# Kernel optimization log

Hardware: AMD Instinct MI355X
Metric: run time of the kernel (lower is better)

## Reference

```python
import jax, jax.numpy as jnp
import numpy as np

INPUT_SIZE = 1024
HIDDEN_SIZE = 1024
BATCH = 8192
MLP_H1, MLP_H2 = 16, 8


def _uniform(key, shape, stdv):
    return jax.random.uniform(key, shape, jnp.float32, -stdv, stdv)


def setup_inputs() -> dict:
    key = jax.random.key(0)
    ks = jax.random.split(key, 20)
    stdv = 1.0 / np.sqrt(HIDDEN_SIZE)
    I, H = INPUT_SIZE, HIDDEN_SIZE
    inp = {
        "x": jax.random.normal(ks[0], (BATCH, I), jnp.float32),
        "h": jax.random.normal(ks[1], (BATCH, H), jnp.float32),
        "c": jax.random.normal(ks[2], (BATCH, H), jnp.float32),
        # gate weights (torch layout: matmul(h, W_h*) + matmul(x, W_x*) + b)
        "W_hi": _uniform(ks[3], (H, H), stdv),
        "W_xi": _uniform(ks[4], (I, H), stdv),
        "b_i": _uniform(ks[5], (H,), stdv),
        "W_hc": _uniform(ks[6], (H, H), stdv),
        "W_xc": _uniform(ks[7], (I, H), stdv),
        "b_c": _uniform(ks[8], (H,), stdv),
        "W_ho": _uniform(ks[9], (H, H), stdv),
        "W_xo": _uniform(ks[10], (I, H), stdv),
        "b_o": _uniform(ks[11], (H,), stdv),
        # forget MLP: (I+H) -> 16 -> 8 -> H, ReLU hidden, sigmoid output
        "W1": _uniform(ks[12], (I + H, MLP_H1), stdv),
        "b1": _uniform(ks[13], (MLP_H1,), stdv),
        "W2": _uniform(ks[14], (MLP_H1, MLP_H2), stdv),
        "b2": _uniform(ks[15], (MLP_H2,), stdv),
        "W3": _uniform(ks[16], (MLP_H2, H), stdv),
        "b3": _uniform(ks[17], (H,), stdv),
    }
    return inp


def reference(x, h, c, W_hi, W_xi, b_i, W_hc, W_xc, b_c, W_ho, W_xo, b_o,
              W1, b1, W2, b2, W3, b3):
    # forget gate via small MLP on concat(x, h)
    xh = jnp.concatenate((x, h), axis=1)           # [B, I+H]
    z = jax.nn.relu(xh @ W1 + b1)                  # [B, 16]
    z = jax.nn.relu(z @ W2 + b2)                   # [B, 8]
    f = jax.nn.sigmoid(z @ W3 + b3)                # [B, H]

    i = jax.nn.sigmoid(h @ W_hi + x @ W_xi + b_i)
    g = jnp.tanh(h @ W_hc + x @ W_xc + b_c)
    o = jax.nn.sigmoid(h @ W_ho + x @ W_xo + b_o)

    c_new = f * c + i * g
    h_new = o * jnp.tanh(c_new)
    return (h_new, c_new, f)
```

## Files before the change

kernel.cpp:

```cpp
#include <hip/hip_runtime.h>
#include <math.h>

#define BATCH 8192
#define HDIM  1024
#define KDIM  2048
#define NDIM  3072

typedef __attribute__((ext_vector_type(8))) short short8;
typedef __attribute__((ext_vector_type(4))) float floatx4;

__device__ __forceinline__ float b2f(unsigned short u) {
  union { unsigned int i; float f; } v; v.i = ((unsigned int)u) << 16; return v.f;
}
__device__ __forceinline__ unsigned short f2b(float f) {
  union { unsigned int i; float f; } v; v.f = f;
  unsigned int r = v.i + 0x7FFFu + ((v.i >> 16) & 1u);
  return (unsigned short)(r >> 16);
}
__device__ __forceinline__ float ldsel(const void* p, size_t i, int isbf) {
  return isbf ? b2f(((const unsigned short*)p)[i]) : ((const float*)p)[i];
}
__device__ __forceinline__ float sigf(float x) { return 1.0f / (1.0f + __expf(-x)); }
__device__ __forceinline__ float tanhfast(float x) {
  float a = __builtin_fabsf(x);
  float t = __expf(-2.f * a);
  float r = (1.f - t) / (1.f + t);
  return copysignf(r, x);
}

__device__ __forceinline__ int detect_bf(const void* x) {
  unsigned int w = ((const unsigned int*)x)[threadIdx.x & 63];
  unsigned short lo = (unsigned short)(w & 0xFFFFu);
  int e = (lo >> 7) & 0xFF;
  bool ok = (e >= 110 && e <= 135) || ((lo & 0x7FFFu) == 0);
  unsigned long long m = __ballot(ok);
  return (__popcll(m) >= 48) ? 1 : 0;
}

__device__ __forceinline__ void gld16(const void* g, void* l) {
  auto gp = reinterpret_cast<__attribute__((address_space(1))) unsigned int*>(
      (unsigned long long)g);
  auto lp = reinterpret_cast<__attribute__((address_space(3))) unsigned int*>(
      (unsigned long long)l);
  __builtin_amdgcn_global_load_lds(gp, lp, 16, 0, 0);
}

__device__ __forceinline__ short8 ld8bf(const void* p, size_t off, int isbf) {
  short8 r;
  if (isbf) {
    r = *(const short8*)((const unsigned short*)p + off);
  } else {
    const float* s = (const float*)p + off;
    float4 a = *(const float4*)(s);
    float4 b = *(const float4*)(s + 4);
    r[0]=(short)f2b(a.x); r[1]=(short)f2b(a.y); r[2]=(short)f2b(a.z); r[3]=(short)f2b(a.w);
    r[4]=(short)f2b(b.x); r[5]=(short)f2b(b.y); r[6]=(short)f2b(b.z); r[7]=(short)f2b(b.w);
  }
  return r;
}

__device__ __forceinline__ void ld8f(const void* p, size_t off, int isbf, float* o) {
  if (isbf) {
    short8 s = *(const short8*)((const unsigned short*)p + off);
#pragma unroll
    for (int j = 0; j < 8; ++j) o[j] = b2f((unsigned short)s[j]);
  } else {
    const float* s = (const float*)p + off;
    float4 a = *(const float4*)(s);
    float4 b = *(const float4*)(s + 4);
    o[0]=a.x; o[1]=a.y; o[2]=a.z; o[3]=a.w;
    o[4]=b.x; o[5]=b.y; o[6]=b.z; o[7]=b.w;
  }
}

__global__ __launch_bounds__(256) void k_pre(
    const void* __restrict__ x, const void* __restrict__ h,
    const void* __restrict__ W1, const void* __restrict__ b1,
    const void* __restrict__ W2, const void* __restrict__ b2,
    const void* __restrict__ wxi, const void* __restrict__ whi,
    const void* __restrict__ wxc, const void* __restrict__ whc,
    const void* __restrict__ wxo, const void* __restrict__ who,
    unsigned short* __restrict__ A, unsigned short* __restrict__ WT,
    float* __restrict__ z2) {
  __shared__ __align__(16) char smem[21888];
  const int isbf = detect_bf(x);
  const int tid = threadIdx.x;
  const int bx = blockIdx.x;

  if (bx < 512) {
    char* tAb = smem;
    char* tBb = smem + 8192;
    float* part = (float*)(smem + 16384);
    float* z1s  = (float*)(smem + 20736);
    const int m0 = bx * 16;
    const int lane = tid & 63;
    const int w = tid >> 6;
    const int q = lane >> 4;
    const int r = lane & 15;
    const int arow = tid >> 4;
    const int ak = (tid & 15) * 16;

    floatx4 acc = {0.f, 0.f, 0.f, 0.f};

    for (int ktile = 0; ktile < 8; ++ktile) {
      const int k0 = ktile * 256;
      const void* src = (k0 < 1024) ? x : h;
      const int klocal = (k0 & 1023) + ak;
      short8 v0 = ld8bf(src, (size_t)(m0 + arow) * 1024 + klocal, isbf);
      short8 v1 = ld8bf(src, (size_t)(m0 + arow) * 1024 + klocal + 8, isbf);
      float wv[16];
      if (isbf) {
        const unsigned short* s = (const unsigned short*)W1 + (size_t)(k0 + tid) * 16;
        short8 s0 = *(const short8*)(s);
        short8 s1 = *(const short8*)(s + 8);
#pragma unroll
        for (int j = 0; j < 8; ++j) { wv[j] = b2f((unsigned short)s0[j]);
                                      wv[8 + j] = b2f((unsigned short)s1[j]); }
      } else {
        const float* s = (const float*)W1 + (size_t)(k0 + tid) * 16;
        float4 a0 = *(const float4*)(s);
        float4 a1 = *(const float4*)(s + 4);
        float4 a2 = *(const float4*)(s + 8);
        float4 a3 = *(const float4*)(s + 12);
        wv[0]=a0.x; wv[1]=a0.y; wv[2]=a0.z; wv[3]=a0.w;
        wv[4]=a1.x; wv[5]=a1.y; wv[6]=a1.z; wv[7]=a1.w;
        wv[8]=a2.x; wv[9]=a2.y; wv[10]=a2.z; wv[11]=a2.w;
        wv[12]=a3.x; wv[13]=a3.y; wv[14]=a3.z; wv[15]=a3.w;
      }
      if (!isbf) {
        unsigned short* Ao = A + (size_t)(m0 + arow) * KDIM + k0 + ak;
        *(short8*)(Ao) = v0;
        *(short8*)(Ao + 8) = v1;
      }
      {
        const int base = arow * 512 + ak * 2;
        const int sw = (arow & 7) << 4;
        *(short8*)(tAb + ((base) ^ sw)) = v0;
        *(short8*)(tAb + ((base + 16) ^ sw)) = v1;
      }
#pragma unroll
      for (int j = 0; j < 16; ++j) {
        *(unsigned short*)(tBb + ((j * 512 + tid * 2) ^ ((j & 7) << 4))) = f2b(wv[j]);
      }
      __syncthreads();
#pragma unroll
      for (int s = 0; s < 2; ++s) {
        const int ks = (w * 2 + s) * 32 + q * 8;
        short8 af = *(const short8*)(tAb + ((r * 512 + ks * 2) ^ ((r & 7) << 4)));
        short8 bf = *(const short8*)(tBb + ((r * 512 + ks * 2) ^ ((r & 7) << 4)));
        acc = __builtin_amdgcn_mfma_f32_16x16x32_bf16(af, bf, acc, 0, 0, 0);
      }
      __syncthreads();
    }
#pragma unroll
    for (int t = 0; t < 4; ++t) part[(w * 16 + q * 4 + t) * 17 + r] = acc[t];
    __syncthreads();
    {
      const int row = tid >> 4;
      const int n = tid & 15;
      float s = part[(0 * 16 + row) * 17 + n] + part[(1 * 16 + row) * 17 + n] +
                part[(2 * 16 + row) * 17 + n] + part[(3 * 16 + row) * 17 + n] +
                ldsel(b1, (size_t)n, isbf);
      z1s[row * 17 + n] = fmaxf(s, 0.f);
    }
    __syncthreads();
    if (tid < 128) {
      const int row = tid >> 3;
      const int p = tid & 7;
      float s = ldsel(b2, (size_t)p, isbf);
#pragma unroll
      for (int nn = 0; nn < 16; ++nn)
        s += z1s[row * 17 + nn] * ldsel(W2, (size_t)nn * 8 + p, isbf);
      z2[(size_t)(m0 + row) * 8 + p] = fmaxf(s, 0.f);
    }
  } else {
    float (*tbuf)[65] = (float(*)[65])smem;
    const int b = bx - 512;
    const int mat = b >> 8;
    const int rem = b & 255;
    const int ti = rem >> 4;
    const int tj = rem & 15;
    const void* Ws[6] = {wxi, whi, wxc, whc, wxo, who};
    const void* W = Ws[mat];
    const int gt = mat >> 1;
    const int half = mat & 1;
    const int rrow = tid >> 3;
    const int c8 = (tid & 7) * 8;
#pragma unroll
    for (int it = 0; it < 2; ++it) {
      int row = it * 32 + rrow;
      size_t off = (size_t)(ti * 64 + row) * 1024 + tj * 64 + c8;
      if (isbf) {
        const unsigned short* s = (const unsigned short*)W + off;
        ushort4 a = *(const ushort4*)(s);
        ushort4 bv = *(const ushort4*)(s + 4);
        tbuf[row][c8+0]=b2f(a.x);  tbuf[row][c8+1]=b2f(a.y);
        tbuf[row][c8+2]=b2f(a.z);  tbuf[row][c8+3]=b2f(a.w);
        tbuf[row][c8+4]=b2f(bv.x); tbuf[row][c8+5]=b2f(bv.y);
        tbuf[row][c8+6]=b2f(bv.z); tbuf[row][c8+7]=b2f(bv.w);
      } else {
        const float* s = (const float*)W + off;
        float4 a = *(const float4*)(s);
        float4 bv = *(const float4*)(s + 4);
        tbuf[row][c8+0]=a.x;  tbuf[row][c8+1]=a.y;  tbuf[row][c8+2]=a.z;  tbuf[row][c8+3]=a.w;
        tbuf[row][c8+4]=bv.x; tbuf[row][c8+5]=bv.y; tbuf[row][c8+6]=bv.z; tbuf[row][c8+7]=bv.w;
      }
    }
    __syncthreads();
#pragma unroll
    for (int it = 0; it < 2; ++it) {
      int nl = it * 32 + rrow;
      int n = gt * 1024 + tj * 64 + nl;
      int kk = half * 1024 + ti * 64 + c8;
      short8 pk;
#pragma unroll
      for (int i = 0; i < 8; ++i) pk[i] = (short)f2b(tbuf[c8 + i][nl]);
      *(short8*)(WT + (size_t)n * KDIM + kk) = pk;
    }
  }
}

__global__ __launch_bounds__(256, 3) void k_gemm(
    const void* __restrict__ x, const void* __restrict__ h,
    const unsigned short* __restrict__ Apack,
    const unsigned short* __restrict__ WT,
    unsigned short* __restrict__ P) {
  const int isbf = detect_bf(x);
  const unsigned short* Ax = isbf ? (const unsigned short*)x : Apack;
  const unsigned short* Ah = isbf ? (const unsigned short*)h : (Apack + 1024);
  const int sA = isbf ? 1024 : 2048;
  __shared__ __align__(16) unsigned short lA[128 * 64];
  __shared__ __align__(16) unsigned short lB[128 * 64];
  const int tid = threadIdx.x;
  const int lane = tid & 63;
  const int wv = tid >> 6;
  const int wm = (wv >> 1) << 6;
  const int wn = (wv & 1) << 6;
  const int lin = blockIdx.y * 24 + blockIdx.x;
  const int swz = ((lin & 7) * 192) + (lin >> 3);
  const int m0 = (swz / 24) << 7;
  const int n0 = (swz % 24) << 7;

  floatx4 acc[4][4];
  const floatx4 fzero = {0.f, 0.f, 0.f, 0.f};
#pragma unroll
  for (int i = 0; i < 4; ++i)
#pragma unroll
    for (int j = 0; j < 4; ++j) acc[i][j] = fzero;

  int rr[4], kk[4];
#pragma unroll
  for (int ps = 0; ps < 4; ++ps) {
    int chunk = ps * 256 + tid;
    rr[ps] = chunk >> 3;
    kk[ps] = (chunk & 7) ^ (rr[ps] & 7);
  }
  const int px0 = (lane >> 4) ^ (lane & 7);
  const int px1 = ((lane >> 4) + 4) ^ (lane & 7);
  const int rowA = wm + (lane & 15);
  const int rowB = wn + (lane & 15);

  for (int kt = 0; kt < KDIM / 64; ++kt) {
    const int k0 = kt * 64;
    const unsigned short* Abase = (k0 < 1024) ? (Ax + k0) : (Ah + (k0 - 1024));
#pragma unroll
    for (int ps = 0; ps < 4; ++ps) {
      const int chunk = ps * 256 + tid;
      gld16(Abase + (size_t)(m0 + rr[ps]) * sA + kk[ps] * 8, lA + chunk * 8);
      gld16(WT + ((size_t)(n0 + rr[ps]) * KDIM + k0 + kk[ps] * 8), lB + chunk * 8);
    }
    __syncthreads();
#pragma unroll
    for (int s = 0; s < 2; ++s) {
      const int px = s ? px1 : px0;
      short8 af[4], bfr[4];
#pragma unroll
      for (int i = 0; i < 4; ++i)
        af[i] = *(const short8*)(lA + ((((rowA + (i << 4)) << 3) + px) << 3));
#pragma unroll
      for (int i = 0; i < 4; ++i)
        bfr[i] = *(const short8*)(lB + ((((rowB + (i << 4)) << 3) + px) << 3));
#pragma unroll
      for (int mi = 0; mi < 4; ++mi)
#pragma unroll
        for (int ni = 0; ni < 4; ++ni)
          acc[mi][ni] = __builtin_amdgcn_mfma_f32_16x16x32_bf16(
              af[mi], bfr[ni], acc[mi][ni], 0, 0, 0);
    }
    __syncthreads();
  }
  const int col = lane & 15;
  const int rq = (lane >> 4) << 2;
#pragma unroll
  for (int mi = 0; mi < 4; ++mi) {
#pragma unroll
    for (int ni = 0; ni < 4; ++ni) {
      const size_t n = (size_t)(n0 + wn + (ni << 4) + col);
#pragma unroll
      for (int t = 0; t < 4; ++t) {
        const size_t m = (size_t)(m0 + wm + (mi << 4) + rq + t);
        P[m * NDIM + n] = f2b(acc[mi][ni][t]);
      }
    }
  }
}

__global__ __launch_bounds__(256) void k_pointwise(
    const unsigned short* __restrict__ P, const void* __restrict__ x,
    const void* __restrict__ cin,
    const void* __restrict__ bi, const void* __restrict__ bc,
    const void* __restrict__ bo, const float* __restrict__ z2,
    const void* __restrict__ W3, const void* __restrict__ b3,
    void* __restrict__ out) {
  const int isbf = detect_bf(x);
  const int tid = threadIdx.x;
  const int n = (tid & 127) * 8;
  const int rhalf = tid >> 7;
  const size_t MH = (size_t)BATCH * HDIM;

  short8 w3p[8];
  float bif[8], bcf[8], bof[8], b3f[8];
  if (isbf) {
#pragma unroll
    for (int j = 0; j < 8; ++j)
      w3p[j] = *(const short8*)((const unsigned short*)W3 + j * 1024 + n);
  } else {
#pragma unroll
    for (int j = 0; j < 8; ++j) {
      const float* s = (const float*)W3 + j * 1024 + n;
      float4 a = *(const float4*)(s);
      float4 b = *(const float4*)(s + 4);
      short8 pk;
      pk[0]=(short)f2b(a.x); pk[1]=(short)f2b(a.y); pk[2]=(short)f2b(a.z); pk[3]=(short)f2b(a.w);
      pk[4]=(short)f2b(b.x); pk[5]=(short)f2b(b.y); pk[6]=(short)f2b(b.z); pk[7]=(short)f2b(b.w);
      w3p[j] = pk;
    }
  }
  ld8f(bi, (size_t)n, isbf, bif);
  ld8f(bc, (size_t)n, isbf, bcf);
  ld8f(bo, (size_t)n, isbf, bof);
  ld8f(b3, (size_t)n, isbf, b3f);

  const size_t mbase = (size_t)blockIdx.x * 4 + rhalf;
#pragma unroll
  for (int rI = 0; rI < 2; ++rI) {
    const size_t m = mbase + rI * 2;
    const size_t idx = m * HDIM + n;
    const unsigned short* pr = P + m * NDIM + n;
    short8 ui = *(const short8*)(pr);
    short8 ug = *(const short8*)(pr + 1024);
    short8 uo = *(const short8*)(pr + 2048);
    float4 za = *(const float4*)(z2 + m * 8);
    float4 zb = *(const float4*)(z2 + m * 8 + 4);
    float zz[8] = {za.x, za.y, za.z, za.w, zb.x, zb.y, zb.z, zb.w};
    float cf[8];
    ld8f(cin, idx, isbf, cf);
    float hn[8], cn[8], ff[8];
#pragma unroll
    for (int t = 0; t < 8; ++t) {
      float f3 = b3f[t];
#pragma unroll
      for (int j = 0; j < 8; ++j) f3 += zz[j] * b2f((unsigned short)w3p[j][t]);
      const float F = sigf(f3);
      const float I = sigf(b2f((unsigned short)ui[t]) + bif[t]);
      const float G = tanhfast(b2f((unsigned short)ug[t]) + bcf[t]);
      const float O = sigf(b2f((unsigned short)uo[t]) + bof[t]);
      const float C = F * cf[t] + I * G;
      ff[t] = F;
      cn[t] = C;
      hn[t] = O * tanhfast(C);
    }
    if (isbf) {
      unsigned short* ob = (unsigned short*)out;
      short8 ph, pc, pf;
#pragma unroll
      for (int t = 0; t < 8; ++t) {
        ph[t] = (short)f2b(hn[t]);
        pc[t] = (short)f2b(cn[t]);
        pf[t] = (short)f2b(ff[t]);
      }
      *(short8*)(ob + idx) = ph;
      *(short8*)(ob + MH + idx) = pc;
      *(short8*)(ob + 2 * MH + idx) = pf;
    } else {
      float* ob = (float*)out;
      *(float4*)(ob + idx)     = make_float4(hn[0], hn[1], hn[2], hn[3]);
      *(float4*)(ob + idx + 4) = make_float4(hn[4], hn[5], hn[6], hn[7]);
      *(float4*)(ob + MH + idx)     = make_float4(cn[0], cn[1], cn[2], cn[3]);
      *(float4*)(ob + MH + idx + 4) = make_float4(cn[4], cn[5], cn[6], cn[7]);
      *(float4*)(ob + 2 * MH + idx)     = make_float4(ff[0], ff[1], ff[2], ff[3]);
      *(float4*)(ob + 2 * MH + idx + 4) = make_float4(ff[4], ff[5], ff[6], ff[7]);
    }
  }
}

extern "C" void kernel_launch(void* const* d_in, const int* in_sizes, int n_in,
                              void* d_out, int out_size, void* d_ws, size_t ws_size,
                              hipStream_t stream) {
  const void* x    = d_in[0];
  const void* h    = d_in[1];
  const void* c    = d_in[2];
  const void* W_hi = d_in[3];
  const void* W_xi = d_in[4];
  const void* b_i  = d_in[5];
  const void* W_hc = d_in[6];
  const void* W_xc = d_in[7];
  const void* b_c  = d_in[8];
  const void* W_ho = d_in[9];
  const void* W_xo = d_in[10];
  const void* b_o  = d_in[11];
  const void* W1   = d_in[12];
  const void* b1   = d_in[13];
  const void* W2   = d_in[14];
  const void* b2   = d_in[15];
  const void* W3   = d_in[16];
  const void* b3   = d_in[17];

  char* ws = (char*)d_ws;
  unsigned short* A   = (unsigned short*)ws;
  unsigned short* WT  = (unsigned short*)(ws + 33554432);
  unsigned short* P   = (unsigned short*)(ws + 46137344);
  float*          z2b = (float*)(ws + 96468992);

  k_pre<<<dim3(2048), dim3(256), 0, stream>>>(x, h, W1, b1, W2, b2,
                                              W_xi, W_hi, W_xc, W_hc, W_xo, W_ho,
                                              A, WT, z2b);
  k_gemm<<<dim3(NDIM / 128, BATCH / 128), dim3(256), 0, stream>>>(x, h, A, WT, P);
  k_pointwise<<<dim3(BATCH / 4), dim3(256), 0, stream>>>(P, x, c, b_i, b_c, b_o,
                                                         z2b, W3, b3, d_out);
}
```

Baseline: 364.4 us.

## Pipeline GEMM with 4-stage LDS ring buffer and 256x128 tiles

The bf16 GEMM kernel now uses 512-thread blocks, each computing a 256x128 output tile. It streams 32-wide K slices through a 4-slot shared-memory ring, so global-to-LDS loads for future slices are issued while the MFMAs run on the current one. Explicit vmcnt waits, raw s_barrier and s_setprio replace the two __syncthreads per K step, and the LDS swizzle changes to match. This is meant to hide global load latency and cut synchronization stalls, at the cost of 96KB of LDS per block, lower occupancy, and dropping the previous block-index swizzle used for L2 locality.

```diff
diff --git a/kernel.cpp b/kernel.cpp
--- a/kernel.cpp
+++ b/kernel.cpp
@@ -220,26 +220,47 @@
   }
 }
 
-__global__ __launch_bounds__(256, 3) void k_gemm(
+__device__ __forceinline__ void stage_a(char* smem, const unsigned short* Ax,
+    const unsigned short* Ah, int sA, int m0, int tid, int n) {
+  const int kb = (n >> 1) * 64 + (n & 1) * 32;
+  const unsigned short* sp = (kb < 1024) ? (Ax + kb) : (Ah + (kb - 1024));
+#pragma unroll
+  for (int j = 0; j < 2; ++j) {
+    const int d = j * 512 + tid;
+    const int row = d >> 2;
+    const int q = (d & 3) ^ ((row >> 1) & 3);
+    gld16(sp + (size_t)(m0 + row) * sA + q * 8,
+          smem + ((n & 3) << 14) + d * 16);
+  }
+}
+__device__ __forceinline__ void stage_b(char* smem, const unsigned short* WT,
+    int n0, int tid, int n) {
+  const int kb = (n >> 1) * 64 + (n & 1) * 32;
+  const int row = tid >> 2;
+  const int q = (tid & 3) ^ ((row >> 1) & 3);
+  gld16(WT + (size_t)(n0 + row) * (size_t)KDIM + kb + q * 8,
+        smem + 65536 + ((n & 3) << 13) + tid * 16);
+}
+
+__global__ __launch_bounds__(512, 2) void k_gemm(
     const void* __restrict__ x, const void* __restrict__ h,
     const unsigned short* __restrict__ Apack,
     const unsigned short* __restrict__ WT,
     unsigned short* __restrict__ P) {
+  __shared__ __align__(16) char smem[98304];
   const int isbf = detect_bf(x);
   const unsigned short* Ax = isbf ? (const unsigned short*)x : Apack;
   const unsigned short* Ah = isbf ? (const unsigned short*)h : (Apack + 1024);
-  const int sA = isbf ? 1024 : 2048;
-  __shared__ __align__(16) unsigned short lA[128 * 64];
-  __shared__ __align__(16) unsigned short lB[128 * 64];
+  const int sA = isbf ? 1024 : KDIM;
   const int tid = threadIdx.x;
   const int lane = tid & 63;
   const int wv = tid >> 6;
   const int wm = (wv >> 1) << 6;
   const int wn = (wv & 1) << 6;
-  const int lin = blockIdx.y * 24 + blockIdx.x;
-  const int swz = ((lin & 7) * 192) + (lin >> 3);
-  const int m0 = (swz / 24) << 7;
-  const int n0 = (swz % 24) << 7;
+  const int m0 = blockIdx.y << 8;
+  const int n0 = blockIdx.x << 7;
+  const int ln15 = lane & 15;
+  const int cp = (((lane >> 4) ^ ((ln15 >> 1) & 3)) & 3) << 4;
 
   floatx4 acc[4][4];
   const floatx4 fzero = {0.f, 0.f, 0.f, 0.f};
@@ -248,48 +269,58 @@
 #pragma unroll
     for (int j = 0; j < 4; ++j) acc[i][j] = fzero;
 
-  int rr[4], kk[4];
-#pragma unroll
-  for (int ps = 0; ps < 4; ++ps) {
-    int chunk = ps * 256 + tid;
-    rr[ps] = chunk >> 3;
-    kk[ps] = (chunk & 7) ^ (rr[ps] & 7);
-  }
-  const int px0 = (lane >> 4) ^ (lane & 7);
-  const int px1 = ((lane >> 4) + 4) ^ (lane & 7);
-  const int rowA = wm + (lane & 15);
-  const int rowB = wn + (lane & 15);
-
-  for (int kt = 0; kt < KDIM / 64; ++kt) {
-    const int k0 = kt * 64;
-    const unsigned short* Abase = (k0 < 1024) ? (Ax + k0) : (Ah + (k0 - 1024));
-#pragma unroll
-    for (int ps = 0; ps < 4; ++ps) {
-      const int chunk = ps * 256 + tid;
-      gld16(Abase + (size_t)(m0 + rr[ps]) * sA + kk[ps] * 8, lA + chunk * 8);
-      gld16(WT + ((size_t)(n0 + rr[ps]) * KDIM + k0 + kk[ps] * 8), lB + chunk * 8);
-    }
-    __syncthreads();
-#pragma unroll
-    for (int s = 0; s < 2; ++s) {
-      const int px = s ? px1 : px0;
-      short8 af[4], bfr[4];
-#pragma unroll
-      for (int i = 0; i < 4; ++i)
-        af[i] = *(const short8*)(lA + ((((rowA + (i << 4)) << 3) + px) << 3));
-#pragma unroll
-      for (int i = 0; i < 4; ++i)
-        bfr[i] = *(const short8*)(lB + ((((rowB + (i << 4)) << 3) + px) << 3));
+  stage_a(smem, Ax, Ah, sA, m0, tid, 0);
+  stage_b(smem, WT, n0, tid, 0);
+  stage_a(smem, Ax, Ah, sA, m0, tid, 1);
+  stage_b(smem, WT, n0, tid, 1);
+  stage_a(smem, Ax, Ah, sA, m0, tid, 2);
+  stage_b(smem, WT, n0, tid, 2);
+  asm volatile("s_waitcnt vmcnt(3)" ::: "memory");
+  __builtin_amdgcn_s_barrier();
+
+  short8 af[4];
+  for (int t = 0; t < 32; ++t) {
+    const int na = 2 * t + 3;
+    const int nb = 2 * t + 4;
+#pragma unroll
+    for (int kh = 0; kh < 2; ++kh) {
+      const int sl = (2 * t + kh) & 3;
+      const char* Ab = smem + (sl << 14);
+      const char* Bb = smem + 65536 + (sl << 13);
+      const int ns = kh ? nb : na;
 #pragma unroll
       for (int mi = 0; mi < 4; ++mi)
-#pragma unroll
-        for (int ni = 0; ni < 4; ++ni)
-          acc[mi][ni] = __builtin_amdgcn_mfma_f32_16x16x32_bf16(
-              af[mi], bfr[ni], acc[mi][ni], 0, 0, 0);
-    }
-    __syncthreads();
-  }
-  const int col = lane & 15;
+        af[mi] = *(const short8*)(Ab + ((wm + mi * 16 + ln15) << 6) + cp);
+      short8 b0 = *(const short8*)(Bb + ((wn + ln15) << 6) + cp);
+      short8 b1 = *(const short8*)(Bb + ((wn + 16 + ln15) << 6) + cp);
+      if (ns <= 63) stage_a(smem, Ax, Ah, sA, m0, tid, ns);
+      __builtin_amdgcn_s_setprio(1);
+#pragma unroll
+      for (int mi = 0; mi < 4; ++mi) {
+        acc[mi][0] = __builtin_amdgcn_mfma_f32_16x16x32_bf16(af[mi], b0, acc[mi][0], 0, 0, 0);
+        acc[mi][1] = __builtin_amdgcn_mfma_f32_16x16x32_bf16(af[mi], b1, acc[mi][1], 0, 0, 0);
+      }
+      __builtin_amdgcn_s_setprio(0);
+      asm volatile("s_barrier" ::: "memory");
+      b0 = *(const short8*)(Bb + ((wn + 32 + ln15) << 6) + cp);
+      b1 = *(const short8*)(Bb + ((wn + 48 + ln15) << 6) + cp);
+      if (ns <= 63) stage_b(smem, WT, n0, tid, ns);
+      __builtin_amdgcn_s_setprio(1);
+#pragma unroll
+      for (int mi = 0; mi < 4; ++mi) {
+        acc[mi][2] = __builtin_amdgcn_mfma_f32_16x16x32_bf16(af[mi], b0, acc[mi][2], 0, 0, 0);
+        acc[mi][3] = __builtin_amdgcn_mfma_f32_16x16x32_bf16(af[mi], b1, acc[mi][3], 0, 0, 0);
+      }
+      __builtin_amdgcn_s_setprio(0);
+      if (kh) {
+        if (t >= 30) asm volatile("s_waitcnt vmcnt(0)" ::: "memory");
+        else         asm volatile("s_waitcnt vmcnt(3)" ::: "memory");
+      }
+      asm volatile("s_barrier" ::: "memory");
+    }
+  }
+
+  const int col = ln15;
   const int rq = (lane >> 4) << 2;
 #pragma unroll
   for (int mi = 0; mi < 4; ++mi) {
@@ -425,7 +456,7 @@
   k_pre<<<dim3(2048), dim3(256), 0, stream>>>(x, h, W1, b1, W2, b2,
                                               W_xi, W_hi, W_xc, W_hc, W_xo, W_ho,
                                               A, WT, z2b);
-  k_gemm<<<dim3(NDIM / 128, BATCH / 128), dim3(256), 0, stream>>>(x, h, A, WT, P);
+  k_gemm<<<dim3(NDIM / 128, BATCH / 256), dim3(512), 0, stream>>>(x, h, A, WT, P);
   k_pointwise<<<dim3(BATCH / 4), dim3(256), 0, stream>>>(P, x, c, b_i, b_c, b_o,
                                                          z2b, W3, b3, d_out);
 }
```

Result: slower. 377.4 us (+3.6%).
